# Kernel tuning notes

Measured on AMD Instinct MI355X. Metric: run time of the kernel, lower is better.

## Reference

```python
import jax, jax.numpy as jnp
import numpy as np

L, H, E, V, BS = 12, 12, 768, 50257, 1024  # layers, heads, n_embd, vocab, block_size
B, T = 2, 1024
D = E // H


def setup_inputs() -> dict:
    key = jax.random.key(0)
    ks = jax.random.split(key, 10)
    s = 0.02
    d = {}
    d["idx"] = jax.random.randint(ks[0], (B, T), 0, V)
    d["targets"] = jax.random.randint(ks[1], (B, T), 0, V)
    # embeddings (wte tied with lm_head)
    d["wte"] = (jax.random.normal(ks[2], (V, E)) * s).astype(jnp.float32)
    d["wpe"] = (jax.random.normal(ks[3], (BS, E)) * s).astype(jnp.float32)
    # stacked per-layer params; Linear weights stored [in, out] (= torch W.T)
    d["ln1_w"] = jnp.ones((L, E), jnp.float32)
    d["ln1_b"] = jnp.zeros((L, E), jnp.float32)
    d["attn_w"] = (jax.random.normal(ks[4], (L, E, 3 * E)) * s).astype(jnp.float32)
    d["attn_b"] = jnp.zeros((L, 3 * E), jnp.float32)
    d["proj_w"] = (jax.random.normal(ks[5], (L, E, E)) * s).astype(jnp.float32)
    d["proj_b"] = jnp.zeros((L, E), jnp.float32)
    d["ln2_w"] = jnp.ones((L, E), jnp.float32)
    d["ln2_b"] = jnp.zeros((L, E), jnp.float32)
    d["fc_w"] = (jax.random.normal(ks[6], (L, E, 4 * E)) * s).astype(jnp.float32)
    d["fc_b"] = jnp.zeros((L, 4 * E), jnp.float32)
    d["fcproj_w"] = (jax.random.normal(ks[7], (L, 4 * E, E)) * s).astype(jnp.float32)
    d["fcproj_b"] = jnp.zeros((L, E), jnp.float32)
    d["lnf_w"] = jnp.ones((E,), jnp.float32)
    d["lnf_b"] = jnp.zeros((E,), jnp.float32)
    return d


def _ln(x, w, b, eps=1e-5):
    m = jnp.mean(x, -1, keepdims=True)
    v = jnp.mean(jnp.square(x - m), -1, keepdims=True)
    return (x - m) * jax.lax.rsqrt(v + eps) * w + b


def _block(x, p, mask):
    l1w, l1b, aw, ab, pw, pb, l2w, l2b, fw, fb, fpw, fpb = p
    Bx, Tx, C = x.shape
    # causal self-attention (explicit QK^T + mask + softmax + AV, as in source)
    qkv = _ln(x, l1w, l1b) @ aw + ab                       # [B,T,3E]
    q, k, v = jnp.split(qkv, 3, axis=-1)
    q = q.reshape(Bx, Tx, H, D).transpose(0, 2, 1, 3)       # [B,H,T,D]
    k = k.reshape(Bx, Tx, H, D).transpose(0, 2, 1, 3)
    v = v.reshape(Bx, Tx, H, D).transpose(0, 2, 1, 3)
    att = jnp.einsum('bhqd,bhkd->bhqk', q, k) * (1.0 / np.sqrt(D))
    att = jnp.where(mask, att, -jnp.inf)
    att = jax.nn.softmax(att, axis=-1)
    y = jnp.einsum('bhqk,bhkd->bhqd', att, v)
    y = y.transpose(0, 2, 1, 3).reshape(Bx, Tx, C)
    x = x + y @ pw + pb
    # MLP with tanh-approx GELU
    h = jax.nn.gelu(_ln(x, l2w, l2b) @ fw + fb, approximate=True)
    x = x + h @ fpw + fpb
    return x


def reference(idx, targets, wte, wpe, ln1_w, ln1_b, attn_w, attn_b, proj_w, proj_b,
              ln2_w, ln2_b, fc_w, fc_b, fcproj_w, fcproj_b, lnf_w, lnf_b):
    Tq = idx.shape[1]
    x = wte[idx] + wpe[:Tq]                                 # [B,T,E]
    mask = jnp.tril(jnp.ones((Tq, Tq), dtype=bool))

    def step(x, p):
        return _block(x, p, mask), None

    layer_params = (ln1_w, ln1_b, attn_w, attn_b, proj_w, proj_b,
                    ln2_w, ln2_b, fc_w, fc_b, fcproj_w, fcproj_b)
    x, _ = jax.lax.scan(step, x, layer_params)
    x = _ln(x, lnf_w, lnf_b)
    logits = x @ wte.T                                      # tied lm_head, [B,T,V]
    logp = jax.nn.log_softmax(logits, axis=-1)
    nll = -jnp.take_along_axis(logp, targets[..., None], axis=-1)[..., 0]
    loss = jnp.mean(nll)
    return logits, loss
```

## Files before the change

### kernel.cpp

```cpp
#include <hip/hip_runtime.h>
#include <hip/hip_bf16.h>
#include <math.h>

#define LNUM 12
#define HNUM 12
#define EDIM 768
#define VDIM 50257
#define BDIM 2
#define TDIM 1024
#define BT (BDIM*TDIM)
#define E3 (3*EDIM)
#define E4 (4*EDIM)
#define NPB (2*((VDIM+127)/128))

typedef __bf16 bf16x8 __attribute__((ext_vector_type(8)));
typedef float f32x4 __attribute__((ext_vector_type(4)));

__device__ __forceinline__ float gelu_f(float x) {
    float u = 0.7978845608028654f * (x + 0.044715f * x * x * x);
    return 0.5f * x * (1.0f + tanhf(u));
}

__device__ __forceinline__ void gl16(const void* g, void* l) {
    __builtin_amdgcn_global_load_lds(
        (const __attribute__((address_space(1))) unsigned int*)g,
        (__attribute__((address_space(3))) unsigned int*)l,
        16, 0, 0);
}

__global__ __launch_bounds__(256) void embed_kernel(
    const int* __restrict__ idx, const float* __restrict__ wte,
    const float* __restrict__ wpe, float* __restrict__ x)
{
    const int row = blockIdx.x;
    const int t = row % TDIM;
    const int tok = idx[row];
    const float* we = wte + (size_t)tok * EDIM;
    const float* pe = wpe + (size_t)t * EDIM;
    float* xr = x + (size_t)row * EDIM;
    for (int e = threadIdx.x; e < EDIM; e += 256) xr[e] = we[e] + pe[e];
}

__global__ __launch_bounds__(256) void ln_kernel(
    const float* __restrict__ in, const float* __restrict__ w,
    const float* __restrict__ b, __bf16* __restrict__ out)
{
    const int row = blockIdx.x, tid = threadIdx.x;
    const float* xr = in + (size_t)row * EDIM;
    float v0 = xr[tid], v1 = xr[tid + 256], v2 = xr[tid + 512];
    float s = v0 + v1 + v2;
    __shared__ float red[8];
    const int lane = tid & 63, wid = tid >> 6;
    #pragma unroll
    for (int off = 32; off; off >>= 1) s += __shfl_xor(s, off);
    if (lane == 0) red[wid] = s;
    __syncthreads();
    const float mean = (red[0] + red[1] + red[2] + red[3]) * (1.0f / EDIM);
    float d0 = v0 - mean, d1 = v1 - mean, d2 = v2 - mean;
    float s2 = d0 * d0 + d1 * d1 + d2 * d2;
    #pragma unroll
    for (int off = 32; off; off >>= 1) s2 += __shfl_xor(s2, off);
    if (lane == 0) red[4 + wid] = s2;
    __syncthreads();
    const float var = (red[4] + red[5] + red[6] + red[7]) * (1.0f / EDIM);
    const float inv = rsqrtf(var + 1e-5f);
    __bf16* orow = out + (size_t)row * EDIM;
    orow[tid]       = (__bf16)(d0 * inv * w[tid]       + b[tid]);
    orow[tid + 256] = (__bf16)(d1 * inv * w[tid + 256] + b[tid + 256]);
    orow[tid + 512] = (__bf16)(d2 * inv * w[tid + 512] + b[tid + 512]);
}

__global__ __launch_bounds__(256) void convt_kernel(
    const float* __restrict__ in, __bf16* __restrict__ out, int K, int N)
{
    in  += (size_t)blockIdx.z * K * N;
    out += (size_t)blockIdx.z * K * N;
    __shared__ float t[32][33];
    const int n0 = blockIdx.x * 32, k0 = blockIdx.y * 32;
    const int tx = threadIdx.x & 31, ty = threadIdx.x >> 5;
    #pragma unroll
    for (int r = ty; r < 32; r += 8)
        t[r][tx] = in[(size_t)(k0 + r) * N + n0 + tx];
    __syncthreads();
    #pragma unroll
    for (int r = ty; r < 32; r += 8)
        out[(size_t)(n0 + r) * K + k0 + tx] = (__bf16)t[tx][r];
}

__global__ __launch_bounds__(256) void cvt_kernel(
    const float* __restrict__ in, __bf16* __restrict__ out, long n4)
{
    for (long i = blockIdx.x * 256L + threadIdx.x; i < n4; i += (long)gridDim.x * 256L) {
        float4 v = ((const float4*)in)[i];
        out[i * 4 + 0] = (__bf16)v.x;
        out[i * 4 + 1] = (__bf16)v.y;
        out[i * 4 + 2] = (__bf16)v.z;
        out[i * 4 + 3] = (__bf16)v.w;
    }
}

template<int BM, int BN, bool BIAS, bool GELU_, bool RES_, bool OUTBF, bool NGUARD, bool LOGITS>
__global__ __launch_bounds__(256) void mgemm(
    const __bf16* __restrict__ A, const __bf16* __restrict__ Bt,
    const float* __restrict__ bias, const float* __restrict__ res,
    void* __restrict__ Cout, float* __restrict__ part, int M, int N, int K)
{
    constexpr int WM = BM / 2, WN = BN / 2;
    constexpr int FM = WM / 16, FN = WN / 16;
    constexpr int rA = BM / 64, rB = BN / 64;
    __shared__ __align__(16) __bf16 As[2 * BM * 32];
    __shared__ __align__(16) __bf16 Bs[2 * BN * 32];
    const int tid = threadIdx.x;
    const int lane = tid & 63;
    const int wave = tid >> 6;
    const int wr = wave >> 1, wc = wave & 1;

    int bm, bn;
    if (LOGITS) {
        const int wg = blockIdx.x;
        bn = (wg & 7) + ((wg >> 7) << 3);
        bm = (wg >> 3) & 15;
        if (bn * 128 >= N) return;
    } else { bm = blockIdx.y; bn = blockIdx.x; }
    const int m0 = bm * BM;
    const int n0 = bn * BN;

    const int srow = tid >> 2;
    const int c0 = (tid & 3) ^ ((srow >> 1) & 3);

    const __bf16* gA = A + (size_t)(m0 + srow) * K + c0 * 8;
    const __bf16* gB[2];
    #pragma unroll
    for (int r = 0; r < rB; ++r) {
        int nr = n0 + srow + r * 64;
        if (NGUARD) nr = nr < N ? nr : N - 1;
        gB[r] = Bt + (size_t)nr * K + c0 * 8;
    }

    const int fr = lane & 15;
    const int g = lane >> 4;
    const int slot = ((g ^ ((lane >> 1) & 3)) << 4);
    const int offA = (wr * WM + fr) * 64 + slot;
    const int offB = (wc * WN + fr) * 64 + slot;

    f32x4 acc[FM][FN];
    #pragma unroll
    for (int i = 0; i < FM; i++)
        #pragma unroll
        for (int j = 0; j < FN; j++) acc[i][j] = (f32x4){0.f, 0.f, 0.f, 0.f};

    const int nt = K >> 5;
    #pragma unroll
    for (int r = 0; r < rA; ++r)
        gl16(gA + (size_t)r * 64 * K, (char*)As + r * 4096 + tid * 16);
    #pragma unroll
    for (int r = 0; r < rB; ++r)
        gl16(gB[r], (char*)Bs + r * 4096 + tid * 16);
    __syncthreads();

    int buf = 0;
    for (int t = 0; t < nt; ++t) {
        if (t + 1 < nt) {
            const int k1 = (t + 1) << 5;
            #pragma unroll
            for (int r = 0; r < rA; ++r)
                gl16(gA + (size_t)r * 64 * K + k1, (char*)As + (buf ^ 1) * (BM * 64) + r * 4096 + tid * 16);
            #pragma unroll
            for (int r = 0; r < rB; ++r)
                gl16(gB[r] + k1, (char*)Bs + (buf ^ 1) * (BN * 64) + r * 4096 + tid * 16);
        }
        const char* pa = (const char*)As + buf * (BM * 64);
        const char* pb = (const char*)Bs + buf * (BN * 64);
        bf16x8 af[FM], bfr[FN];
        #pragma unroll
        for (int i = 0; i < FM; i++)
            af[i] = *(const bf16x8*)(pa + offA + i * 1024);
        #pragma unroll
        for (int j = 0; j < FN; j++)
            bfr[j] = *(const bf16x8*)(pb + offB + j * 1024);
        #pragma unroll
        for (int i = 0; i < FM; i++)
            #pragma unroll
            for (int j = 0; j < FN; j++)
                acc[i][j] = __builtin_amdgcn_mfma_f32_16x16x32_bf16(af[i], bfr[j], acc[i][j], 0, 0, 0);
        __syncthreads();
        buf ^= 1;
    }

    const int crow = g * 4;
    if (LOGITS) {
        const int bn2 = bn * 2 + wc;
        #pragma unroll
        for (int i = 0; i < FM; i++) {
            #pragma unroll
            for (int r = 0; r < 4; r++) {
                const int m = m0 + wr * WM + i * 16 + crow + r;
                float se = 0.f;
                #pragma unroll
                for (int j = 0; j < FN; j++) {
                    const int n = n0 + wc * WN + j * 16 + fr;
                    if (!NGUARD || n < N) {
                        float v = acc[i][j][r];
                        ((float*)Cout)[(size_t)m * N + n] = v;
                        se += __expf(v);
                    }
                }
                se += __shfl_xor(se, 1); se += __shfl_xor(se, 2);
                se += __shfl_xor(se, 4); se += __shfl_xor(se, 8);
                if (fr == 0) part[(size_t)m * NPB + bn2] = se;
            }
        }
    } else {
        #pragma unroll
        for (int i = 0; i < FM; i++) {
            #pragma unroll
            for (int r = 0; r < 4; r++) {
                const int m = m0 + wr * WM + i * 16 + crow + r;
                #pragma unroll
                for (int j = 0; j < FN; j++) {
                    const int n = n0 + wc * WN + j * 16 + fr;
                    if (!NGUARD || n < N) {
                        float v = acc[i][j][r];
                        if (BIAS) v += bias[n];
                        if (GELU_) v = gelu_f(v);
                        if (RES_) v += res[(size_t)m * N + n];
                        if (OUTBF) ((__bf16*)Cout)[(size_t)m * N + n] = (__bf16)v;
                        else       ((float*)Cout)[(size_t)m * N + n] = v;
                    }
                }
            }
        }
    }
}

__global__ __launch_bounds__(256) void fattn_kernel(
    const __bf16* __restrict__ qkv, __bf16* __restrict__ y)
{
    const int bq = blockIdx.x, h = blockIdx.y, b = blockIdx.z;
    const int tid = threadIdx.x, lane = tid & 63, w = tid >> 6;
    const int fr = lane & 15, g = lane >> 4;

    __shared__ __align__(16) __bf16 Ks[64 * 64];
    __shared__ __align__(16) __bf16 Vt[64 * 64];
    __shared__ __align__(16) __bf16 Ps[4][16 * 64];

    const __bf16* base = qkv + (size_t)b * TDIM * E3;
    const int q0w = bq * 64 + w * 16;

    bf16x8 qf[2];
    {
        const __bf16* qp = base + (size_t)(q0w + fr) * E3 + h * 64 + g * 8;
        qf[0] = *(const bf16x8*)qp;
        qf[1] = *(const bf16x8*)(qp + 32);
    }

    const int r0 = tid >> 3, ch = tid & 7;
    bf16x8 kr[2], vr[2];

    #pragma unroll
    for (int it = 0; it < 2; ++it) {
        const int row = it * 32 + r0;
        const __bf16* gp = base + (size_t)row * E3 + EDIM + h * 64 + ch * 8;
        kr[it] = *(const bf16x8*)gp;
        vr[it] = *(const bf16x8*)(gp + EDIM);
    }
    #pragma unroll
    for (int it = 0; it < 2; ++it) {
        const int row = it * 32 + r0;
        *(bf16x8*)(Ks + row * 64 + ((ch ^ (row & 7)) << 3)) = kr[it];
        #pragma unroll
        for (int j = 0; j < 8; ++j) {
            const int d = ch * 8 + j;
            const int key = ((d >> 3) ^ d) & 7;
            Vt[d * 64 + ((((row >> 3) ^ key) << 3) + (row & 7))] = vr[it][j];
        }
    }
    __syncthreads();

    float m[4] = {-1e30f, -1e30f, -1e30f, -1e30f};
    float l[4] = {0.f, 0.f, 0.f, 0.f};
    f32x4 acc[4];
    #pragma unroll
    for (int jd = 0; jd < 4; ++jd) acc[jd] = (f32x4){0.f, 0.f, 0.f, 0.f};

    for (int kt = 0; kt <= bq; ++kt) {
        if (kt < bq) {
            const int k1 = (kt + 1) * 64;
            #pragma unroll
            for (int it = 0; it < 2; ++it) {
                const int row = it * 32 + r0;
                const __bf16* gp = base + (size_t)(k1 + row) * E3 + EDIM + h * 64 + ch * 8;
                kr[it] = *(const bf16x8*)gp;
                vr[it] = *(const bf16x8*)(gp + EDIM);
            }
        }

        const int k0 = kt * 64;
        f32x4 s[4];
        #pragma unroll
        for (int jf = 0; jf < 4; ++jf) {
            const int krow = jf * 16 + fr;
            f32x4 sv = (f32x4){0.f, 0.f, 0.f, 0.f};
            #pragma unroll
            for (int kc = 0; kc < 2; ++kc) {
                bf16x8 kf = *(const bf16x8*)(Ks + krow * 64 + (((kc * 4 + g) ^ (fr & 7)) << 3));
                sv = __builtin_amdgcn_mfma_f32_16x16x32_bf16(qf[kc], kf, sv, 0, 0, 0);
            }
            s[jf] = sv;
        }
        #pragma unroll
        for (int jf = 0; jf < 4; ++jf)
            #pragma unroll
            for (int r = 0; r < 4; ++r) s[jf][r] *= 0.125f;
        if (kt == bq) {
            #pragma unroll
            for (int jf = 0; jf < 4; ++jf) {
                const int k = k0 + jf * 16 + fr;
                #pragma unroll
                for (int r = 0; r < 4; ++r) {
                    const int q = q0w + g * 4 + r;
                    if (k > q) s[jf][r] = -1e30f;
                }
            }
        }

        #pragma unroll
        for (int r = 0; r < 4; ++r) {
            float mx = fmaxf(fmaxf(s[0][r], s[1][r]), fmaxf(s[2][r], s[3][r]));
            mx = fmaxf(mx, __shfl_xor(mx, 1));
            mx = fmaxf(mx, __shfl_xor(mx, 2));
            mx = fmaxf(mx, __shfl_xor(mx, 4));
            mx = fmaxf(mx, __shfl_xor(mx, 8));
            const float mn = fmaxf(m[r], mx);
            const float sc2 = __expf(m[r] - mn);
            m[r] = mn;
            float rs = 0.f;
            #pragma unroll
            for (int jf = 0; jf < 4; ++jf) {
                const float p = __expf(s[jf][r] - mn);
                s[jf][r] = p;
                rs += p;
            }
            rs += __shfl_xor(rs, 1);
            rs += __shfl_xor(rs, 2);
            rs += __shfl_xor(rs, 4);
            rs += __shfl_xor(rs, 8);
            l[r] = l[r] * sc2 + rs;
            #pragma unroll
            for (int jd = 0; jd < 4; ++jd) acc[jd][r] *= sc2;
        }

        __bf16* pw = &Ps[w][0];
        #pragma unroll
        for (int jf = 0; jf < 4; ++jf) {
            const int chp = jf * 2 + (fr >> 3);
            #pragma unroll
            for (int r = 0; r < 4; ++r) {
                const int row = g * 4 + r;
                pw[row * 64 + (((chp ^ (row & 7)) << 3) + (fr & 7))] = (__bf16)s[jf][r];
            }
        }
        asm volatile("s_waitcnt lgkmcnt(0)" ::: "memory");
        bf16x8 pa[2];
        #pragma unroll
        for (int kc = 0; kc < 2; ++kc)
            pa[kc] = *(const bf16x8*)(pw + fr * 64 + (((kc * 4 + g) ^ (fr & 7)) << 3));

        #pragma unroll
        for (int jd = 0; jd < 4; ++jd) {
            const int d = jd * 16 + fr;
            const int key = ((d >> 3) ^ d) & 7;
            #pragma unroll
            for (int kc = 0; kc < 2; ++kc) {
                bf16x8 vf = *(const bf16x8*)(Vt + d * 64 + (((kc * 4 + g) ^ key) << 3));
                acc[jd] = __builtin_amdgcn_mfma_f32_16x16x32_bf16(pa[kc], vf, acc[jd], 0, 0, 0);
            }
        }

        if (kt < bq) {
            __syncthreads();
            #pragma unroll
            for (int it = 0; it < 2; ++it) {
                const int row = it * 32 + r0;
                *(bf16x8*)(Ks + row * 64 + ((ch ^ (row & 7)) << 3)) = kr[it];
                #pragma unroll
                for (int j = 0; j < 8; ++j) {
                    const int d = ch * 8 + j;
                    const int key = ((d >> 3) ^ d) & 7;
                    Vt[d * 64 + ((((row >> 3) ^ key) << 3) + (row & 7))] = vr[it][j];
                }
            }
            __syncthreads();
        }
    }

    #pragma unroll
    for (int r = 0; r < 4; ++r) {
        const float inv = 1.0f / l[r];
        const int q = q0w + g * 4 + r;
        __bf16* yp = y + ((size_t)(b * TDIM + q)) * EDIM + h * 64;
        #pragma unroll
        for (int jd = 0; jd < 4; ++jd)
            yp[jd * 16 + fr] = (__bf16)(acc[jd][r] * inv);
    }
}

__global__ __launch_bounds__(256) void lsefin_kernel(
    const float* __restrict__ part, const float* __restrict__ logits,
    const int* __restrict__ targets, float* __restrict__ rr)
{
    const int row = blockIdx.x, tid = threadIdx.x;
    float s = 0.f;
    for (int j = tid; j < NPB; j += 256) s += part[(size_t)row * NPB + j];
    #pragma unroll
    for (int off = 32; off; off >>= 1) s += __shfl_xor(s, off);
    __shared__ float red[4];
    if ((tid & 63) == 0) red[tid >> 6] = s;
    __syncthreads();
    if (tid == 0) {
        float S = red[0] + red[1] + red[2] + red[3];
        rr[row] = logf(S) - logits[(size_t)row * VDIM + targets[row]];
    }
}

__global__ __launch_bounds__(256) void loss_reduce_kernel(
    const float* __restrict__ rr, float* __restrict__ out)
{
    const int tid = threadIdx.x;
    float s = 0.f;
    for (int i = tid; i < BT; i += 256) s += rr[i];
    #pragma unroll
    for (int off = 32; off; off >>= 1) s += __shfl_xor(s, off);
    __shared__ float red[4];
    if ((tid & 63) == 0) red[tid >> 6] = s;
    __syncthreads();
    if (tid == 0) out[0] = (red[0] + red[1] + red[2] + red[3]) * (1.0f / BT);
}

extern "C" void kernel_launch(void* const* d_in, const int* in_sizes, int n_in,
                              void* d_out, int out_size, void* d_ws, size_t ws_size,
                              hipStream_t stream)
{
    const int*   idx     = (const int*)d_in[0];
    const int*   targets = (const int*)d_in[1];
    const float* wte     = (const float*)d_in[2];
    const float* wpe     = (const float*)d_in[3];
    const float* ln1_w   = (const float*)d_in[4];
    const float* ln1_b   = (const float*)d_in[5];
    const float* attn_w  = (const float*)d_in[6];
    const float* attn_b  = (const float*)d_in[7];
    const float* proj_w  = (const float*)d_in[8];
    const float* proj_b  = (const float*)d_in[9];
    const float* ln2_w   = (const float*)d_in[10];
    const float* ln2_b   = (const float*)d_in[11];
    const float* fc_w    = (const float*)d_in[12];
    const float* fc_b    = (const float*)d_in[13];
    const float* fcp_w   = (const float*)d_in[14];
    const float* fcp_b   = (const float*)d_in[15];
    const float* lnf_w   = (const float*)d_in[16];
    const float* lnf_b   = (const float*)d_in[17];

    float* logits = (float*)d_out;

    const size_t slq = (size_t)EDIM * E3, slp = (size_t)EDIM * EDIM;
    const size_t slf = (size_t)EDIM * E4, slfp = (size_t)E4 * EDIM;

    char* wp = (char*)d_ws;
    float*  x     = (float*)wp;   wp += (size_t)BT * EDIM * 4;
    __bf16* qkvb  = (__bf16*)wp;  wp += (size_t)BT * E3 * 2;
    __bf16* xnbf  = (__bf16*)wp;  wp += (size_t)BT * EDIM * 2;
    __bf16* ybf   = (__bf16*)wp;  wp += (size_t)BT * EDIM * 2;
    __bf16* hbf   = (__bf16*)wp;  wp += (size_t)BT * E4 * 2;
    __bf16* wteb  = (__bf16*)wp;  wp += (size_t)VDIM * EDIM * 2;
    float*  part  = (float*)wp;   wp += (size_t)BT * NPB * 4;
    float*  rr    = (float*)wp;   wp += (size_t)BT * 4;
    __bf16* wqkvb = (__bf16*)wp;

    const size_t wbytes_all = (slq + slp + slf + slfp) * 2 * LNUM;
    const size_t used = (size_t)(wp - (char*)d_ws);
    const bool big = ws_size >= used + wbytes_all;
    const size_t L = big ? LNUM : 1;
    __bf16* wprjb = wqkvb + slq * L;
    __bf16* wfcb  = wprjb + slp * L;
    __bf16* wfpb  = wfcb  + slf * L;

    embed_kernel<<<BT, 256, 0, stream>>>(idx, wte, wpe, x);
    cvt_kernel<<<2048, 256, 0, stream>>>(wte, wteb, (long)VDIM * EDIM / 4);

    if (big) {
        convt_kernel<<<dim3(E3 / 32, EDIM / 32, LNUM), 256, 0, stream>>>(attn_w, wqkvb, EDIM, E3);
        convt_kernel<<<dim3(EDIM / 32, EDIM / 32, LNUM), 256, 0, stream>>>(proj_w, wprjb, EDIM, EDIM);
        convt_kernel<<<dim3(E4 / 32, EDIM / 32, LNUM), 256, 0, stream>>>(fc_w, wfcb, EDIM, E4);
        convt_kernel<<<dim3(EDIM / 32, E4 / 32, LNUM), 256, 0, stream>>>(fcp_w, wfpb, E4, EDIM);
    }

    for (int l = 0; l < LNUM; ++l) {
        const __bf16* wq = wqkvb + (big ? (size_t)l * slq : 0);
        const __bf16* wpj = wprjb + (big ? (size_t)l * slp : 0);
        const __bf16* wf = wfcb + (big ? (size_t)l * slf : 0);
        const __bf16* wfp = wfpb + (big ? (size_t)l * slfp : 0);

        ln_kernel<<<BT, 256, 0, stream>>>(x, ln1_w + (size_t)l * EDIM,
                                          ln1_b + (size_t)l * EDIM, xnbf);
        if (!big)
            convt_kernel<<<dim3(E3 / 32, EDIM / 32), 256, 0, stream>>>(
                attn_w + (size_t)l * slq, (__bf16*)wq, EDIM, E3);
        mgemm<128, 128, true, false, false, true, false, false>
            <<<dim3(E3 / 128, BT / 128), 256, 0, stream>>>(
            xnbf, wq, attn_b + (size_t)l * E3, nullptr, qkvb, nullptr, BT, E3, EDIM);
        fattn_kernel<<<dim3(TDIM / 64, HNUM, BDIM), 256, 0, stream>>>(qkvb, ybf);
        if (!big)
            convt_kernel<<<dim3(EDIM / 32, EDIM / 32), 256, 0, stream>>>(
                proj_w + (size_t)l * slp, (__bf16*)wpj, EDIM, EDIM);
        mgemm<64, 64, true, false, true, false, false, false>
            <<<dim3(EDIM / 64, BT / 64), 256, 0, stream>>>(
            ybf, wpj, proj_b + (size_t)l * EDIM, x, x, nullptr, BT, EDIM, EDIM);
        ln_kernel<<<BT, 256, 0, stream>>>(x, ln2_w + (size_t)l * EDIM,
                                          ln2_b + (size_t)l * EDIM, xnbf);
        if (!big)
            convt_kernel<<<dim3(E4 / 32, EDIM / 32), 256, 0, stream>>>(
                fc_w + (size_t)l * slf, (__bf16*)wf, EDIM, E4);
        mgemm<128, 128, true, true, false, true, false, false>
            <<<dim3(E4 / 128, BT / 128), 256, 0, stream>>>(
            xnbf, wf, fc_b + (size_t)l * E4, nullptr, hbf, nullptr, BT, E4, EDIM);
        if (!big)
            convt_kernel<<<dim3(EDIM / 32, E4 / 32), 256, 0, stream>>>(
                fcp_w + (size_t)l * slfp, (__bf16*)wfp, E4, EDIM);
        mgemm<64, 64, true, false, true, false, false, false>
            <<<dim3(EDIM / 64, BT / 64), 256, 0, stream>>>(
            hbf, wfp, fcp_b + (size_t)l * EDIM, x, x, nullptr, BT, EDIM, E4);
    }

    ln_kernel<<<BT, 256, 0, stream>>>(x, lnf_w, lnf_b, xnbf);
    mgemm<128, 128, false, false, false, false, true, true>
        <<<dim3(16 * 400), 256, 0, stream>>>(
        xnbf, wteb, nullptr, nullptr, logits, part, BT, VDIM, EDIM);
    lsefin_kernel<<<BT, 256, 0, stream>>>(part, logits, targets, rr);
    loss_reduce_kernel<<<1, 256, 0, stream>>>(rr, logits + (size_t)BT * VDIM);
}
```

Measured before the change: 2.356 ms.

## Triple-buffer GEMM K-loop and stage logits epilogue through LDS for vector stores

```diff
diff --git a/kernel.cpp b/kernel.cpp
--- a/kernel.cpp
+++ b/kernel.cpp
@@ -108,8 +108,8 @@
     constexpr int WM = BM / 2, WN = BN / 2;
     constexpr int FM = WM / 16, FN = WN / 16;
     constexpr int rA = BM / 64, rB = BN / 64;
-    __shared__ __align__(16) __bf16 As[2 * BM * 32];
-    __shared__ __align__(16) __bf16 Bs[2 * BN * 32];
+    __shared__ __align__(16) __bf16 As[3 * BM * 32];
+    __shared__ __align__(16) __bf16 Bs[3 * BN * 32];
     const int tid = threadIdx.x;
     const int lane = tid & 63;
     const int wave = tid >> 6;
@@ -150,27 +150,32 @@
         for (int j = 0; j < FN; j++) acc[i][j] = (f32x4){0.f, 0.f, 0.f, 0.f};
 
     const int nt = K >> 5;
-    #pragma unroll
-    for (int r = 0; r < rA; ++r)
-        gl16(gA + (size_t)r * 64 * K, (char*)As + r * 4096 + tid * 16);
-    #pragma unroll
-    for (int r = 0; r < rB; ++r)
-        gl16(gB[r], (char*)Bs + r * 4096 + tid * 16);
-    __syncthreads();
-
-    int buf = 0;
+
+    auto stage = [&](int kk, int b) {
+        #pragma unroll
+        for (int r = 0; r < rA; ++r)
+            gl16(gA + (size_t)r * 64 * K + kk, (char*)As + b * (BM * 64) + r * 4096 + tid * 16);
+        #pragma unroll
+        for (int r = 0; r < rB; ++r)
+            gl16(gB[r] + kk, (char*)Bs + b * (BN * 64) + r * 4096 + tid * 16);
+    };
+
+    stage(0, 0);
+    if (nt > 1) stage(32, 1);
+
+    int b0 = 0, b1 = 1, b2 = 2;
     for (int t = 0; t < nt; ++t) {
         if (t + 1 < nt) {
-            const int k1 = (t + 1) << 5;
-            #pragma unroll
-            for (int r = 0; r < rA; ++r)
-                gl16(gA + (size_t)r * 64 * K + k1, (char*)As + (buf ^ 1) * (BM * 64) + r * 4096 + tid * 16);
-            #pragma unroll
-            for (int r = 0; r < rB; ++r)
-                gl16(gB[r] + k1, (char*)Bs + (buf ^ 1) * (BN * 64) + r * 4096 + tid * 16);
-        }
-        const char* pa = (const char*)As + buf * (BM * 64);
-        const char* pb = (const char*)Bs + buf * (BN * 64);
+            if constexpr (rA + rB == 4) asm volatile("s_waitcnt vmcnt(4)" ::: "memory");
+            else                        asm volatile("s_waitcnt vmcnt(2)" ::: "memory");
+        } else {
+            asm volatile("s_waitcnt vmcnt(0)" ::: "memory");
+        }
+        asm volatile("s_barrier" ::: "memory");
+        if (t + 2 < nt) stage((t + 2) << 5, b2);
+
+        const char* pa = (const char*)As + b0 * (BM * 64);
+        const char* pb = (const char*)Bs + b0 * (BN * 64);
         bf16x8 af[FM], bfr[FN];
         #pragma unroll
         for (int i = 0; i < FM; i++)
@@ -183,8 +188,7 @@
             #pragma unroll
             for (int j = 0; j < FN; j++)
                 acc[i][j] = __builtin_amdgcn_mfma_f32_16x16x32_bf16(af[i], bfr[j], acc[i][j], 0, 0, 0);
-        __syncthreads();
-        buf ^= 1;
+        const int tmp = b0; b0 = b1; b1 = b2; b2 = tmp;
     }
 
     const int crow = g * 4;
@@ -199,15 +203,37 @@
                 #pragma unroll
                 for (int j = 0; j < FN; j++) {
                     const int n = n0 + wc * WN + j * 16 + fr;
-                    if (!NGUARD || n < N) {
-                        float v = acc[i][j][r];
-                        ((float*)Cout)[(size_t)m * N + n] = v;
-                        se += __expf(v);
-                    }
+                    if (n < N) se += __expf(acc[i][j][r]);
                 }
                 se += __shfl_xor(se, 1); se += __shfl_xor(se, 2);
                 se += __shfl_xor(se, 4); se += __shfl_xor(se, 8);
                 if (fr == 0) part[(size_t)m * NPB + bn2] = se;
+            }
+        }
+        __syncthreads();
+        float* lds = (float*)((char*)As + wave * (16 * 68 * 4));
+        const bool full = (n0 + BN <= N);
+        const int rw0 = lane >> 4, cl = (lane & 15) * 4;
+        #pragma unroll
+        for (int i = 0; i < FM; i++) {
+            #pragma unroll
+            for (int j = 0; j < FN; j++)
+                #pragma unroll
+                for (int r = 0; r < 4; r++)
+                    lds[(crow + r) * 68 + j * 16 + fr] = acc[i][j][r];
+            #pragma unroll
+            for (int q = 0; q < 4; q++) {
+                const int rw = q * 4 + rw0;
+                float4 v = *(const float4*)&lds[rw * 68 + cl];
+                const int m = m0 + wr * WM + i * 16 + rw;
+                const int n = n0 + wc * WN + cl;
+                if (full) {
+                    *(float4*)&((float*)Cout)[(size_t)m * N + n] = v;
+                } else {
+                    #pragma unroll
+                    for (int e = 0; e < 4; e++)
+                        if (n + e < N) ((float*)Cout)[(size_t)m * N + n + e] = (&v.x)[e];
+                }
             }
         }
     } else {
```

After: 2.436 ms. +3.4%, slower.

## Triple-buffer GEMM LDS pipeline with explicit vmcnt waits and configurable BK

Applied to the files above, without the earlier changes.

```diff
diff --git a/kernel.cpp b/kernel.cpp
--- a/kernel.cpp
+++ b/kernel.cpp
@@ -99,7 +99,7 @@
     }
 }
 
-template<int BM, int BN, bool BIAS, bool GELU_, bool RES_, bool OUTBF, bool NGUARD, bool LOGITS>
+template<int BM, int BN, int BK, bool BIAS, bool GELU_, bool RES_, bool OUTBF, bool NGUARD, bool LOGITS>
 __global__ __launch_bounds__(256) void mgemm(
     const __bf16* __restrict__ A, const __bf16* __restrict__ Bt,
     const float* __restrict__ bias, const float* __restrict__ res,
@@ -107,9 +107,13 @@
 {
     constexpr int WM = BM / 2, WN = BN / 2;
     constexpr int FM = WM / 16, FN = WN / 16;
-    constexpr int rA = BM / 64, rB = BN / 64;
-    __shared__ __align__(16) __bf16 As[2 * BM * 32];
-    __shared__ __align__(16) __bf16 Bs[2 * BN * 32];
+    constexpr int KS = BK / 32;
+    constexpr int TB = BM * BK * 2;
+    constexpr int rA = TB / 4096, rB = (BN * BK * 2) / 4096;
+    constexpr int RPI = 2048 / BK;
+    constexpr int CPR = BK / 8;
+    __shared__ __align__(16) __bf16 As[3 * BM * BK];
+    __shared__ __align__(16) __bf16 Bs[3 * BN * BK];
     const int tid = threadIdx.x;
     const int lane = tid & 63;
     const int wave = tid >> 6;
@@ -120,28 +124,27 @@
         const int wg = blockIdx.x;
         bn = (wg & 7) + ((wg >> 7) << 3);
         bm = (wg >> 3) & 15;
-        if (bn * 128 >= N) return;
+        if (bn * BN >= N) return;
     } else { bm = blockIdx.y; bn = blockIdx.x; }
     const int m0 = bm * BM;
     const int n0 = bn * BN;
 
-    const int srow = tid >> 2;
-    const int c0 = (tid & 3) ^ ((srow >> 1) & 3);
+    const int srow = tid / CPR;
+    const int skey = (BK == 32) ? ((srow >> 1) & 3) : (srow & 7);
+    const int c0 = (tid % CPR) ^ skey;
 
     const __bf16* gA = A + (size_t)(m0 + srow) * K + c0 * 8;
-    const __bf16* gB[2];
+    const __bf16* gB[rB];
     #pragma unroll
     for (int r = 0; r < rB; ++r) {
-        int nr = n0 + srow + r * 64;
+        int nr = n0 + srow + r * RPI;
         if (NGUARD) nr = nr < N ? nr : N - 1;
         gB[r] = Bt + (size_t)nr * K + c0 * 8;
     }
 
     const int fr = lane & 15;
     const int g = lane >> 4;
-    const int slot = ((g ^ ((lane >> 1) & 3)) << 4);
-    const int offA = (wr * WM + fr) * 64 + slot;
-    const int offB = (wc * WN + fr) * 64 + slot;
+    const int fkey = (BK == 32) ? ((fr >> 1) & 3) : (fr & 7);
 
     f32x4 acc[FM][FN];
     #pragma unroll
@@ -149,42 +152,54 @@
         #pragma unroll
         for (int j = 0; j < FN; j++) acc[i][j] = (f32x4){0.f, 0.f, 0.f, 0.f};
 
-    const int nt = K >> 5;
-    #pragma unroll
-    for (int r = 0; r < rA; ++r)
-        gl16(gA + (size_t)r * 64 * K, (char*)As + r * 4096 + tid * 16);
-    #pragma unroll
-    for (int r = 0; r < rB; ++r)
-        gl16(gB[r], (char*)Bs + r * 4096 + tid * 16);
-    __syncthreads();
-
-    int buf = 0;
+    const int nt = K / BK;
+
+    auto stage = [&](int kk, int b) {
+        #pragma unroll
+        for (int r = 0; r < rA; ++r)
+            gl16(gA + (size_t)r * RPI * K + kk, (char*)As + b * TB + r * 4096 + tid * 16);
+        #pragma unroll
+        for (int r = 0; r < rB; ++r)
+            gl16(gB[r] + kk, (char*)Bs + b * TB + r * 4096 + tid * 16);
+    };
+
+    stage(0, 0);
+    if (nt > 1) stage(BK, 1);
+
+    int b0 = 0, b1 = 1, b2 = 2;
     for (int t = 0; t < nt; ++t) {
         if (t + 1 < nt) {
-            const int k1 = (t + 1) << 5;
-            #pragma unroll
-            for (int r = 0; r < rA; ++r)
-                gl16(gA + (size_t)r * 64 * K + k1, (char*)As + (buf ^ 1) * (BM * 64) + r * 4096 + tid * 16);
-            #pragma unroll
-            for (int r = 0; r < rB; ++r)
-                gl16(gB[r] + k1, (char*)Bs + (buf ^ 1) * (BN * 64) + r * 4096 + tid * 16);
-        }
-        const char* pa = (const char*)As + buf * (BM * 64);
-        const char* pb = (const char*)Bs + buf * (BN * 64);
-        bf16x8 af[FM], bfr[FN];
+            static_assert(rA + rB == 4, "vmcnt literal assumes 4 loads/stage");
+            asm volatile("s_waitcnt vmcnt(4)" ::: "memory");
+        } else {
+            asm volatile("s_waitcnt vmcnt(0)" ::: "memory");
+        }
+        asm volatile("s_barrier" ::: "memory");
+        if (t + 2 < nt) stage((t + 2) * BK, b2);
+
+        const char* pa = (const char*)As + b0 * TB;
+        const char* pb = (const char*)Bs + b0 * TB;
+        bf16x8 af[FM][KS], bfr[FN][KS];
         #pragma unroll
         for (int i = 0; i < FM; i++)
-            af[i] = *(const bf16x8*)(pa + offA + i * 1024);
+            #pragma unroll
+            for (int kc = 0; kc < KS; kc++)
+                af[i][kc] = *(const bf16x8*)(pa + (wr * WM + i * 16 + fr) * (2 * BK)
+                                                + (((kc * 4 + g) ^ fkey) << 4));
         #pragma unroll
         for (int j = 0; j < FN; j++)
-            bfr[j] = *(const bf16x8*)(pb + offB + j * 1024);
-        #pragma unroll
-        for (int i = 0; i < FM; i++)
-            #pragma unroll
-            for (int j = 0; j < FN; j++)
-                acc[i][j] = __builtin_amdgcn_mfma_f32_16x16x32_bf16(af[i], bfr[j], acc[i][j], 0, 0, 0);
-        __syncthreads();
-        buf ^= 1;
+            #pragma unroll
+            for (int kc = 0; kc < KS; kc++)
+                bfr[j][kc] = *(const bf16x8*)(pb + (wc * WN + j * 16 + fr) * (2 * BK)
+                                                 + (((kc * 4 + g) ^ fkey) << 4));
+        #pragma unroll
+        for (int kc = 0; kc < KS; kc++)
+            #pragma unroll
+            for (int i = 0; i < FM; i++)
+                #pragma unroll
+                for (int j = 0; j < FN; j++)
+                    acc[i][j] = __builtin_amdgcn_mfma_f32_16x16x32_bf16(af[i][kc], bfr[j][kc], acc[i][j], 0, 0, 0);
+        const int tmp = b0; b0 = b1; b1 = b2; b2 = tmp;
     }
 
     const int crow = g * 4;
@@ -199,7 +214,7 @@
                 #pragma unroll
                 for (int j = 0; j < FN; j++) {
                     const int n = n0 + wc * WN + j * 16 + fr;
-                    if (!NGUARD || n < N) {
+                    if (n < N) {
                         float v = acc[i][j][r];
                         ((float*)Cout)[(size_t)m * N + n] = v;
                         se += __expf(v);
@@ -505,14 +520,14 @@
         if (!big)
             convt_kernel<<<dim3(E3 / 32, EDIM / 32), 256, 0, stream>>>(
                 attn_w + (size_t)l * slq, (__bf16*)wq, EDIM, E3);
-        mgemm<128, 128, true, false, false, true, false, false>
+        mgemm<128, 128, 32, true, false, false, true, false, false>
             <<<dim3(E3 / 128, BT / 128), 256, 0, stream>>>(
             xnbf, wq, attn_b + (size_t)l * E3, nullptr, qkvb, nullptr, BT, E3, EDIM);
         fattn_kernel<<<dim3(TDIM / 64, HNUM, BDIM), 256, 0, stream>>>(qkvb, ybf);
         if (!big)
             convt_kernel<<<dim3(EDIM / 32, EDIM / 32), 256, 0, stream>>>(
                 proj_w + (size_t)l * slp, (__bf16*)wpj, EDIM, EDIM);
-        mgemm<64, 64, true, false, true, false, false, false>
+        mgemm<64, 64, 64, true, false, true, false, false, false>
             <<<dim3(EDIM / 64, BT / 64), 256, 0, stream>>>(
             ybf, wpj, proj_b + (size_t)l * EDIM, x, x, nullptr, BT, EDIM, EDIM);
         ln_kernel<<<BT, 256, 0, stream>>>(x, ln2_w + (size_t)l * EDIM,
@@ -520,19 +535,19 @@
         if (!big)
             convt_kernel<<<dim3(E4 / 32, EDIM / 32), 256, 0, stream>>>(
                 fc_w + (size_t)l * slf, (__bf16*)wf, EDIM, E4);
-        mgemm<128, 128, true, true, false, true, false, false>
+        mgemm<128, 128, 32, true, true, false, true, false, false>
             <<<dim3(E4 / 128, BT / 128), 256, 0, stream>>>(
             xnbf, wf, fc_b + (size_t)l * E4, nullptr, hbf, nullptr, BT, E4, EDIM);
         if (!big)
             convt_kernel<<<dim3(EDIM / 32, E4 / 32), 256, 0, stream>>>(
                 fcp_w + (size_t)l * slfp, (__bf16*)wfp, E4, EDIM);
-        mgemm<64, 64, true, false, true, false, false, false>
+        mgemm<64, 64, 64, true, false, true, false, false, false>
             <<<dim3(EDIM / 64, BT / 64), 256, 0, stream>>>(
             hbf, wfp, fcp_b + (size_t)l * EDIM, x, x, nullptr, BT, EDIM, E4);
     }
 
     ln_kernel<<<BT, 256, 0, stream>>>(x, lnf_w, lnf_b, xnbf);
-    mgemm<128, 128, false, false, false, false, true, true>
+    mgemm<128, 128, 32, false, false, false, false, true, true>
         <<<dim3(16 * 400), 256, 0, stream>>>(
         xnbf, wteb, nullptr, nullptr, logits, part, BT, VDIM, EDIM);
     lsefin_kernel<<<BT, 256, 0, stream>>>(part, logits, targets, rr);
```

Measured after the change: 2.264 ms. -3.9%, faster.
